# Kernel tuning notes

Hardware: AMD Instinct MI355X
Metric: run time of the kernel (lower is better)

Reference implementation:

```python
import jax, jax.numpy as jnp
import numpy as np

HID = 64; N_LAYERS = 4; N_HEADS = 4; HEAD_DIM = 16; INTER = 32; MAXP = 1024; EPS = 1e-12


def setup_inputs() -> dict:
    key = jax.random.key(0)
    ks = iter(jax.random.split(key, 32))
    rn = lambda shape, s=0.02: jax.random.normal(next(ks), shape, jnp.float32) * s
    B, L = 32, 1024
    return {
        "features": jax.random.normal(next(ks), (B, L, HID), jnp.float32),
        "Wq": rn((N_LAYERS, HID, HID)), "bq": jnp.zeros((N_LAYERS, HID), jnp.float32),
        "Wk": rn((N_LAYERS, HID, HID)), "bk": jnp.zeros((N_LAYERS, HID), jnp.float32),
        "Wv": rn((N_LAYERS, HID, HID)), "bv": jnp.zeros((N_LAYERS, HID), jnp.float32),
        "Wo": rn((N_LAYERS, HID, HID)), "bo": jnp.zeros((N_LAYERS, HID), jnp.float32),
        "ln1_g": jnp.ones((N_LAYERS, HID), jnp.float32), "ln1_b": jnp.zeros((N_LAYERS, HID), jnp.float32),
        "Wi": rn((N_LAYERS, HID, INTER)), "bi": jnp.zeros((N_LAYERS, INTER), jnp.float32),
        "Wd": rn((N_LAYERS, INTER, HID)), "bd": jnp.zeros((N_LAYERS, HID), jnp.float32),
        "ln2_g": jnp.ones((N_LAYERS, HID), jnp.float32), "ln2_b": jnp.zeros((N_LAYERS, HID), jnp.float32),
        "rel_emb": rn((N_LAYERS, 2 * MAXP - 1, HEAD_DIM)),
        "fc_w": rn((HID, 6)), "fc_b": jnp.zeros((6,), jnp.float32),
    }


def _ln(x, g, b):
    m = jnp.mean(x, axis=-1, keepdims=True)
    v = jnp.mean((x - m) ** 2, axis=-1, keepdims=True)
    return (x - m) / jnp.sqrt(v + EPS) * g + b


def reference(features, Wq, bq, Wk, bk, Wv, bv, Wo, bo, ln1_g, ln1_b,
              Wi, bi, Wd, bd, ln2_g, ln2_b, rel_emb, fc_w, fc_b):
    B, L, _ = features.shape
    pos = jnp.arange(L)
    dist_idx = pos[:, None] - pos[None, :] + (MAXP - 1)  # [L, L] in [0, 2*MAXP-2]
    scale = np.float32(1.0 / np.sqrt(HEAD_DIM))

    def heads(t):  # [B,L,HID] -> [B,H,L,D]
        return t.reshape(B, L, N_HEADS, HEAD_DIM).transpose(0, 2, 1, 3)

    x = features
    for i in range(N_LAYERS):
        q = heads(x @ Wq[i] + bq[i])
        k = heads(x @ Wk[i] + bk[i])
        v = heads(x @ Wv[i] + bv[i])
        scores = jnp.einsum("bhld,bhrd->bhlr", q, k)
        pe = rel_emb[i][dist_idx]  # [L, L, D] relative_key positional embedding
        scores = scores + jnp.einsum("bhld,lrd->bhlr", q, pe)
        probs = jax.nn.softmax(scores * scale, axis=-1)
        ctx = jnp.einsum("bhlr,bhrd->bhld", probs, v).transpose(0, 2, 1, 3).reshape(B, L, HID)
        x = _ln(ctx @ Wo[i] + bo[i] + x, ln1_g[i], ln1_b[i])
        inter = jax.nn.gelu(x @ Wi[i] + bi[i], approximate=False)
        x = _ln(inter @ Wd[i] + bd[i] + x, ln2_g[i], ln2_b[i])
    return (x @ fc_w + fc_b)[:, 1:, :]
```

## Files before the change

kernel.cpp:

```cpp
#include <hip/hip_runtime.h>
#include <math.h>

static constexpr int Bc = 32;
static constexpr int Lc = 1024;

typedef _Float16 f16x4 __attribute__((ext_vector_type(4)));
typedef __fp16   h16x2 __attribute__((ext_vector_type(2)));
typedef float    f32x4 __attribute__((ext_vector_type(4)));

#define MFMA16(a, b, c) __builtin_amdgcn_mfma_f32_16x16x16f16((a), (b), (c), 0, 0, 0)

#if __has_builtin(__builtin_amdgcn_exp2f)
#define EXP2(x) __builtin_amdgcn_exp2f(x)
#else
#define EXP2(x) exp2f(x)
#endif

__global__ __launch_bounds__(256) void prep_kernel(
    const float* __restrict__ features, const float* __restrict__ rel,
    const float* __restrict__ Wq, const float* __restrict__ Wk,
    const float* __restrict__ Wv, const float* __restrict__ Wo,
    const float* __restrict__ Wi, const float* __restrict__ Wd,
    _Float16* __restrict__ xh, _Float16* __restrict__ relh,
    _Float16* __restrict__ wt)
{
    int i = blockIdx.x * 256 + threadIdx.x;
    {
        float4 v = ((const float4*)features)[i];
        h16x2 a = __builtin_amdgcn_cvt_pkrtz(v.x, v.y);
        h16x2 b = __builtin_amdgcn_cvt_pkrtz(v.z, v.w);
        f16x4 o; o[0] = a[0]; o[1] = a[1]; o[2] = b[0]; o[3] = b[1];
        ((f16x4*)xh)[i] = o;
    }
    if (i < 32752) {
        float4 v = ((const float4*)rel)[i];
        h16x2 a = __builtin_amdgcn_cvt_pkrtz(v.x, v.y);
        h16x2 b = __builtin_amdgcn_cvt_pkrtz(v.z, v.w);
        f16x4 o; o[0] = a[0]; o[1] = a[1]; o[2] = b[0]; o[3] = b[1];
        ((f16x4*)relh)[i] = o;
    }
    if (i < 65536) {
        int which = i >> 14, r = i & 16383;
        int m = r >> 12, k = (r >> 6) & 63, c = r & 63;
        const float* src = which == 0 ? Wq : which == 1 ? Wk : which == 2 ? Wv : Wo;
        wt[which * 16384 + m * 4096 + c * 64 + k] = (_Float16)src[r];
    } else if (i < 73728) {
        int r = i - 65536;
        int m = r >> 11, k = (r >> 5) & 63, c = r & 31;
        wt[65536 + m * 2048 + c * 64 + k] = (_Float16)Wi[r];
    } else if (i < 81920) {
        int r = i - 73728;
        int m = r >> 11, k = (r >> 6) & 31, c = r & 63;
        wt[73728 + m * 2048 + c * 32 + k] = (_Float16)Wd[r];
    }
}

__global__ __launch_bounds__(256) void qkv_kernel(
    const _Float16* __restrict__ xh,
    const _Float16* __restrict__ qT, const _Float16* __restrict__ kT,
    const _Float16* __restrict__ vT,
    const float* __restrict__ bq, const float* __restrict__ bk,
    const float* __restrict__ bv,
    _Float16* __restrict__ qo, _Float16* __restrict__ ko, _Float16* __restrict__ vt)
{
    const int t = threadIdx.x, wv = t >> 6, lane = t & 63, lo = lane & 15, hi = lane >> 4;
    const int row0 = blockIdx.x * 64 + wv * 16;
    const int b = row0 >> 10, l0 = row0 & 1023;

    f16x4 a[4];
    #pragma unroll
    for (int kk = 0; kk < 4; kk++)
        a[kk] = *(const f16x4*)(xh + (row0 + lo) * 64 + kk * 16 + 4 * hi);

    #pragma unroll
    for (int m = 0; m < 3; m++) {
        const _Float16* WT = m == 0 ? qT : m == 1 ? kT : vT;
        const float* bias  = m == 0 ? bq : m == 1 ? bk : bv;
        #pragma unroll
        for (int h = 0; h < 4; h++) {
            float bb = bias[h * 16 + lo];
            f32x4 acc = { bb, bb, bb, bb };
            #pragma unroll
            for (int kk = 0; kk < 4; kk++) {
                f16x4 bf = *(const f16x4*)(WT + (h * 16 + lo) * 64 + kk * 16 + 4 * hi);
                acc = MFMA16(a[kk], bf, acc);
            }
            int bh = b * 4 + h;
            if (m < 2) {
                _Float16* dst = (m == 0 ? qo : ko) + (bh * Lc + l0 + 4 * hi) * 16 + lo;
                dst[0]  = (_Float16)acc[0];
                dst[16] = (_Float16)acc[1];
                dst[32] = (_Float16)acc[2];
                dst[48] = (_Float16)acc[3];
            } else {
                h16x2 p0 = __builtin_amdgcn_cvt_pkrtz(acc[0], acc[1]);
                h16x2 p1 = __builtin_amdgcn_cvt_pkrtz(acc[2], acc[3]);
                f16x4 o; o[0] = p0[0]; o[1] = p0[1]; o[2] = p1[0]; o[3] = p1[1];
                *(f16x4*)(vt + (bh * 16 + lo) * Lc + l0 + 4 * hi) = o;
            }
        }
    }
}

__global__ __launch_bounds__(256) void layer_kernel(
    const _Float16* __restrict__ qg, const _Float16* __restrict__ kg,
    const _Float16* __restrict__ vtg, const _Float16* __restrict__ relh,
    const float* __restrict__ resid,
    const _Float16* __restrict__ woT, const float* __restrict__ bo,
    const float* __restrict__ g1, const float* __restrict__ b1,
    const _Float16* __restrict__ wiT, const float* __restrict__ bi,
    const _Float16* __restrict__ wdT, const float* __restrict__ bd,
    const float* __restrict__ g2, const float* __restrict__ b2,
    float* __restrict__ xout,
    int doq,
    const _Float16* __restrict__ qT, const _Float16* __restrict__ kT,
    const _Float16* __restrict__ vT,
    const float* __restrict__ bq, const float* __restrict__ bk,
    const float* __restrict__ bv,
    _Float16* __restrict__ qo, _Float16* __restrict__ ko, _Float16* __restrict__ vo)
{
    __shared__ float Tmem[4 * 3328];
    const int tid = threadIdx.x;
    const int wv = tid >> 6, lane = tid & 63;
    const int b  = blockIdx.x & 31;
    const int l0 = (blockIdx.x >> 5) * 64;
    const int bh = b * 4 + wv;
    const int lo = lane & 15, hi = lane >> 4;
    float* wbase = Tmem + wv * 3328;

    {
        const _Float16 qscale = (_Float16)0.36067376022224085f;
        f16x4 qf[4];
        #pragma unroll
        for (int i = 0; i < 4; i++) {
            qf[i] = *(const f16x4*)(qg + (bh * Lc + l0 + 16 * i + lo) * 16 + 4 * hi);
            #pragma unroll
            for (int j = 0; j < 4; j++) qf[i][j] *= qscale;
        }

        const int o = 12 + lo - 4 * hi;

        float* wrE[4]; float* wrO[4]; const float* rdE[4]; const float* rdO[4];
        #pragma unroll
        for (int i = 0; i < 4; i++) {
            float* ring = wbase + i * 832;
            const int phiE = 16 * (i & 1);
            const int phiO = 16 - phiE;
            wrE[i] = ring + lo * 52 + phiE + 4 * hi;
            wrO[i] = ring + lo * 52 + phiO + 4 * hi;
            rdE[i] = ring + lo * 52 + phiE + o;
            rdO[i] = ring + lo * 52 + phiO + o;
        }

        const _Float16* rbase = relh + 4 * hi;
        auto ldrel = [&](int row) {
            row = row > 2046 ? 2046 : row;
            return *(const f16x4*)(rbase + row * 16);
        };
        auto t_store = [&](f16x4 rf, f16x4 q, float* wr, bool mir) {
            f32x4 z = { 0.f, 0.f, 0.f, 0.f };
            f32x4 tt = MFMA16(rf, q, z);
            *(f32x4*)(wr) = tt;
            if (mir) *(f32x4*)(wr + 32) = tt;
        };

        f16x4 P[6];
        #pragma unroll
        for (int k = 0; k < 6; k++) P[k] = ldrel(l0 + 16 * k + lo);
        #pragma unroll
        for (int i = 0; i < 4; i++) {
            t_store(P[i],     qf[i], wrE[i], (i & 1) == 0);
            t_store(P[i + 1], qf[i], wrO[i], (i & 1) == 1);
        }
        f16x4 rc0 = P[2], rc1 = P[3], rc2 = P[4], rc3 = P[5];
        int rrow = l0 + 96 + lo;

        f32x4 si[4];
        #pragma unroll
        for (int i = 0; i < 4; i++) {
            const float* rd = rdE[i];
            si[i][0] = rd[3]; si[i][1] = rd[2]; si[i][2] = rd[1]; si[i][3] = rd[0];
        }

        const _Float16* kp = kg  + (bh * Lc + 1008 + lo) * 16 + 4 * hi;
        const _Float16* vp = vtg + (bh * 16 + lo) * Lc + 1008 + 4 * hi;
        f16x4 kf0 = *(const f16x4*)kp;
        f16x4 vf0 = *(const f16x4*)vp;
        kp -= 256; vp -= 16;
        f16x4 kf1 = *(const f16x4*)kp;
        f16x4 vf1 = *(const f16x4*)vp;

        f32x4 ot[4], d[4];
        #pragma unroll
        for (int i = 0; i < 4; i++) {
            ot[i] = f32x4{ 0.f, 0.f, 0.f, 0.f };
            d[i]  = f32x4{ 0.f, 0.f, 0.f, 0.f };
        }

        #pragma unroll 2
        for (int t = 0; t < 64; ++t) {
            kp -= 256; vp -= 16;
            f16x4 kf2 = *(const f16x4*)kp;
            f16x4 vf2 = *(const f16x4*)vp;
            f16x4 r4 = ldrel(rrow); rrow += 16;

            f32x4 s[4];
            #pragma unroll
            for (int i = 0; i < 4; i++)
                s[i] = MFMA16(kf0, qf[i], si[i]);

            float e[4][4];
            #pragma unroll
            for (int i = 0; i < 4; i++)
                #pragma unroll
                for (int j = 0; j < 4; j++) {
                    e[i][j] = EXP2(s[i][j]);
                    d[i][j] += e[i][j];
                }

            t_store(rc0, qf[0], (t & 1) ? wrO[0] : wrE[0], (t & 1) == 0);
            t_store(rc1, qf[1], (t & 1) ? wrO[1] : wrE[1], (t & 1) == 1);
            t_store(rc2, qf[2], (t & 1) ? wrO[2] : wrE[2], (t & 1) == 0);
            t_store(rc3, qf[3], (t & 1) ? wrO[3] : wrE[3], (t & 1) == 1);

            #pragma unroll
            for (int i = 0; i < 4; i++) {
                const float* rd = (t & 1) ? rdE[i] : rdO[i];
                si[i][0] = rd[3]; si[i][1] = rd[2]; si[i][2] = rd[1]; si[i][3] = rd[0];
            }

            #pragma unroll
            for (int i = 0; i < 4; i++) {
                h16x2 pa = __builtin_amdgcn_cvt_pkrtz(e[i][0], e[i][1]);
                h16x2 pb = __builtin_amdgcn_cvt_pkrtz(e[i][2], e[i][3]);
                f16x4 pf; pf[0] = pa[0]; pf[1] = pa[1]; pf[2] = pb[0]; pf[3] = pb[1];
                ot[i] = MFMA16(vf0, pf, ot[i]);
            }

            kf0 = kf1; kf1 = kf2;
            vf0 = vf1; vf1 = vf2;
            rc0 = rc1; rc1 = rc2; rc2 = rc3; rc3 = r4;
        }

        _Float16* ctxw = (_Float16*)wbase;
        #pragma unroll
        for (int i = 0; i < 4; i++) {
            float den = (d[i][0] + d[i][1]) + (d[i][2] + d[i][3]);
            den += __shfl_xor(den, 16);
            den += __shfl_xor(den, 32);
            const float inv = 1.f / den;
            h16x2 o0 = __builtin_amdgcn_cvt_pkrtz(ot[i][0] * inv, ot[i][1] * inv);
            h16x2 o1 = __builtin_amdgcn_cvt_pkrtz(ot[i][2] * inv, ot[i][3] * inv);
            f16x4 o4; o4[0] = o0[0]; o4[1] = o0[1]; o4[2] = o1[0]; o4[3] = o1[1];
            *(f16x4*)(ctxw + (16 * i + lo) * 16 + 4 * hi) = o4;
        }
    }
    __syncthreads();

    const _Float16* ctxs = (const _Float16*)Tmem;
    const int row0g = b * Lc + l0 + wv * 16;

    f16x4 a[4];
    #pragma unroll
    for (int kk = 0; kk < 4; kk++)
        a[kk] = *(const f16x4*)(ctxs + kk * 6656 + (wv * 16 + lo) * 16 + 4 * hi);

    float c1[4][4];
    #pragma unroll
    for (int w = 0; w < 4; w++) {
        float bb = bo[w * 16 + lo];
        f32x4 acc;
        #pragma unroll
        for (int j = 0; j < 4; j++)
            acc[j] = bb + resid[(row0g + 4 * hi + j) * 64 + w * 16 + lo];
        #pragma unroll
        for (int kk = 0; kk < 4; kk++) {
            f16x4 bf = *(const f16x4*)(woT + (w * 16 + lo) * 64 + kk * 16 + 4 * hi);
            acc = MFMA16(a[kk], bf, acc);
        }
        #pragma unroll
        for (int j = 0; j < 4; j++) c1[w][j] = acc[j];
    }

    float x1[4][4];
    {
        float gg[4], bb2[4];
        #pragma unroll
        for (int w = 0; w < 4; w++) { gg[w] = g1[w * 16 + lo]; bb2[w] = b1[w * 16 + lo]; }
        #pragma unroll
        for (int j = 0; j < 4; j++) {
            float s = c1[0][j] + c1[1][j] + c1[2][j] + c1[3][j];
            float q = c1[0][j]*c1[0][j] + c1[1][j]*c1[1][j] + c1[2][j]*c1[2][j] + c1[3][j]*c1[3][j];
            #pragma unroll
            for (int off = 1; off < 16; off <<= 1) { s += __shfl_xor(s, off); q += __shfl_xor(q, off); }
            float m  = s * (1.f / 64.f);
            float vr = q * (1.f / 64.f) - m * m;
            float rs = rsqrtf(vr + 1e-12f);
            #pragma unroll
            for (int w = 0; w < 4; w++) x1[w][j] = (c1[w][j] - m) * rs * gg[w] + bb2[w];
        }
    }

    _Float16* xsp = (_Float16*)(wbase + 512);
    _Float16* isp = (_Float16*)(wbase + 512 + 544);

    #pragma unroll
    for (int w = 0; w < 4; w++)
        #pragma unroll
        for (int j = 0; j < 4; j++)
            xsp[(4 * hi + j) * 68 + w * 16 + lo] = (_Float16)x1[w][j];
    f16x4 a2[4];
    #pragma unroll
    for (int kk = 0; kk < 4; kk++)
        a2[kk] = *(const f16x4*)(xsp + lo * 68 + kk * 16 + 4 * hi);

    float it[2][4];
    #pragma unroll
    for (int w = 0; w < 2; w++) {
        float bb = bi[w * 16 + lo];
        f32x4 acc = { bb, bb, bb, bb };
        #pragma unroll
        for (int kk = 0; kk < 4; kk++) {
            f16x4 bf = *(const f16x4*)(wiT + (w * 16 + lo) * 64 + kk * 16 + 4 * hi);
            acc = MFMA16(a2[kk], bf, acc);
        }
        #pragma unroll
        for (int j = 0; j < 4; j++) {
            float v = acc[j];
            it[w][j] = 0.5f * v * (1.f + erff(v * 0.70710678118654752f));
        }
    }

    #pragma unroll
    for (int w = 0; w < 2; w++)
        #pragma unroll
        for (int j = 0; j < 4; j++)
            isp[(4 * hi + j) * 36 + w * 16 + lo] = (_Float16)it[w][j];
    f16x4 a3[2];
    #pragma unroll
    for (int kk = 0; kk < 2; kk++)
        a3[kk] = *(const f16x4*)(isp + lo * 36 + kk * 16 + 4 * hi);

    float c2[4][4];
    #pragma unroll
    for (int w = 0; w < 4; w++) {
        float bb = bd[w * 16 + lo];
        f32x4 acc;
        #pragma unroll
        for (int j = 0; j < 4; j++) acc[j] = bb + x1[w][j];
        #pragma unroll
        for (int kk = 0; kk < 2; kk++) {
            f16x4 bf = *(const f16x4*)(wdT + (w * 16 + lo) * 32 + kk * 16 + 4 * hi);
            acc = MFMA16(a3[kk], bf, acc);
        }
        #pragma unroll
        for (int j = 0; j < 4; j++) c2[w][j] = acc[j];
    }

    float x2[4][4];
    {
        float gg[4], bb2[4];
        #pragma unroll
        for (int w = 0; w < 4; w++) { gg[w] = g2[w * 16 + lo]; bb2[w] = b2[w * 16 + lo]; }
        #pragma unroll
        for (int j = 0; j < 4; j++) {
            float s = c2[0][j] + c2[1][j] + c2[2][j] + c2[3][j];
            float q = c2[0][j]*c2[0][j] + c2[1][j]*c2[1][j] + c2[2][j]*c2[2][j] + c2[3][j]*c2[3][j];
            #pragma unroll
            for (int off = 1; off < 16; off <<= 1) { s += __shfl_xor(s, off); q += __shfl_xor(q, off); }
            float m  = s * (1.f / 64.f);
            float vr = q * (1.f / 64.f) - m * m;
            float rs = rsqrtf(vr + 1e-12f);
            #pragma unroll
            for (int w = 0; w < 4; w++) {
                float xv = (c2[w][j] - m) * rs * gg[w] + bb2[w];
                x2[w][j] = xv;
                xout[(row0g + 4 * hi + j) * 64 + w * 16 + lo] = xv;
            }
        }
    }

    if (!doq) return;

    #pragma unroll
    for (int w = 0; w < 4; w++)
        #pragma unroll
        for (int j = 0; j < 4; j++)
            xsp[(4 * hi + j) * 68 + w * 16 + lo] = (_Float16)x2[w][j];
    f16x4 aq[4];
    #pragma unroll
    for (int kk = 0; kk < 4; kk++)
        aq[kk] = *(const f16x4*)(xsp + lo * 68 + kk * 16 + 4 * hi);

    const int bb_ = row0g >> 10, l0q = row0g & 1023;
    #pragma unroll
    for (int m = 0; m < 3; m++) {
        const _Float16* WT = m == 0 ? qT : m == 1 ? kT : vT;
        const float* bias  = m == 0 ? bq : m == 1 ? bk : bv;
        #pragma unroll
        for (int h = 0; h < 4; h++) {
            float bb = bias[h * 16 + lo];
            f32x4 acc = { bb, bb, bb, bb };
            #pragma unroll
            for (int kk = 0; kk < 4; kk++) {
                f16x4 bf = *(const f16x4*)(WT + (h * 16 + lo) * 64 + kk * 16 + 4 * hi);
                acc = MFMA16(aq[kk], bf, acc);
            }
            int bhn = bb_ * 4 + h;
            if (m < 2) {
                _Float16* dst = (m == 0 ? qo : ko) + (bhn * Lc + l0q + 4 * hi) * 16 + lo;
                dst[0]  = (_Float16)acc[0];
                dst[16] = (_Float16)acc[1];
                dst[32] = (_Float16)acc[2];
                dst[48] = (_Float16)acc[3];
            } else {
                h16x2 p0 = __builtin_amdgcn_cvt_pkrtz(acc[0], acc[1]);
                h16x2 p1 = __builtin_amdgcn_cvt_pkrtz(acc[2], acc[3]);
                f16x4 o; o[0] = p0[0]; o[1] = p0[1]; o[2] = p1[0]; o[3] = p1[1];
                *(f16x4*)(vo + (bhn * 16 + lo) * Lc + l0q + 4 * hi) = o;
            }
        }
    }
}

__global__ __launch_bounds__(256) void final_kernel(
    const float* __restrict__ x, const float* __restrict__ fcw,
    const float* __restrict__ fcb, float* __restrict__ out)
{
    int idx = blockIdx.x * 256 + threadIdx.x;
    if (idx >= Bc * 1023 * 6) return;
    int j = idx % 6;
    int rest = idx / 6;
    int l = rest % 1023 + 1;
    int b = rest / 1023;
    const float* xr = x + (b * Lc + l) * 64;
    float acc = fcb[j];
    for (int k = 0; k < 64; ++k) acc += xr[k] * fcw[k * 6 + j];
    out[idx] = acc;
}

extern "C" void kernel_launch(void* const* d_in, const int* in_sizes, int n_in,
                              void* d_out, int out_size, void* d_ws, size_t ws_size,
                              hipStream_t stream)
{
    (void)in_sizes; (void)n_in; (void)out_size; (void)ws_size;
    const float* features = (const float*)d_in[0];
    const float* Wq  = (const float*)d_in[1];
    const float* bq  = (const float*)d_in[2];
    const float* Wk  = (const float*)d_in[3];
    const float* bk  = (const float*)d_in[4];
    const float* Wv  = (const float*)d_in[5];
    const float* bv  = (const float*)d_in[6];
    const float* Wo  = (const float*)d_in[7];
    const float* bo  = (const float*)d_in[8];
    const float* g1  = (const float*)d_in[9];
    const float* b1  = (const float*)d_in[10];
    const float* Wi  = (const float*)d_in[11];
    const float* bi  = (const float*)d_in[12];
    const float* Wd  = (const float*)d_in[13];
    const float* bd  = (const float*)d_in[14];
    const float* g2  = (const float*)d_in[15];
    const float* b2  = (const float*)d_in[16];
    const float* rel = (const float*)d_in[17];
    const float* fcw = (const float*)d_in[18];
    const float* fcb = (const float*)d_in[19];
    float* out = (float*)d_out;

    char* ws = (char*)d_ws;
    float*    xbuf = (float*)(ws);
    _Float16* qh1  = (_Float16*)(ws + ( 8u << 20));
    _Float16* xh   = qh1;
    _Float16* kh1  = (_Float16*)(ws + (12u << 20));
    _Float16* vt1  = (_Float16*)(ws + (16u << 20));
    _Float16* qh0  = (_Float16*)(ws + (20u << 20));
    _Float16* kh0  = (_Float16*)(ws + (24u << 20));
    _Float16* vt0  = (_Float16*)(ws + (28u << 20));
    _Float16* relh = (_Float16*)(ws + (32u << 20));
    _Float16* wt   = (_Float16*)(ws + (32u << 20) + (512u << 10));

    prep_kernel<<<2048, 256, 0, stream>>>(features, rel, Wq, Wk, Wv, Wo, Wi, Wd,
                                          xh, relh, wt);
    qkv_kernel<<<512, 256, 0, stream>>>(xh,
        wt, wt + 16384, wt + 32768, bq, bk, bv, qh0, kh0, vt0);

    for (int i = 0; i < 4; ++i) {
        const float* resid = (i == 0) ? features : xbuf;
        const int ni = (i < 3) ? (i + 1) : 3;
        const _Float16* qin = (i & 1) ? qh1 : qh0;
        const _Float16* kin = (i & 1) ? kh1 : kh0;
        const _Float16* vin = (i & 1) ? vt1 : vt0;
        _Float16* qout = (i & 1) ? qh0 : qh1;
        _Float16* kout = (i & 1) ? kh0 : kh1;
        _Float16* vout = (i & 1) ? vt0 : vt1;

        layer_kernel<<<512, 256, 0, stream>>>(qin, kin, vin,
            relh + i * 2047 * 16, resid,
            wt + 49152 + i * 4096, bo + i * 64, g1 + i * 64, b1 + i * 64,
            wt + 65536 + i * 2048, bi + i * 32,
            wt + 73728 + i * 2048, bd + i * 64, g2 + i * 64, b2 + i * 64,
            xbuf,
            (i < 3) ? 1 : 0,
            wt + ni * 4096, wt + 16384 + ni * 4096, wt + 32768 + ni * 4096,
            bq + ni * 64, bk + ni * 64, bv + ni * 64,
            qout, kout, vout);
    }
    final_kernel<<<768, 256, 0, stream>>>(xbuf, fcw, fcb, out);
}
```

Measured before the change: 262.8 us.

## Halve query rows per attention block to double grid size

Each layer block now handles 32 query rows instead of 64, so each wave carries two query tiles instead of four, shared memory is halved, and the grid grows from 512 to 1024 blocks. The aim is better occupancy and more parallelism on the many CUs, with lower register and LDS pressure per block. The cost is twice the K/V and relative-embedding streaming per query, less MFMA work per loaded K/V fragment, and only two of four waves doing the post-attention MLP/projection phase.

Measured after the change: 291.0 us. +10.7%, slower.

```diff
diff --git a/kernel.cpp b/kernel.cpp
--- a/kernel.cpp
+++ b/kernel.cpp
@@ -119,20 +119,20 @@
     const float* __restrict__ bv,
     _Float16* __restrict__ qo, _Float16* __restrict__ ko, _Float16* __restrict__ vo)
 {
-    __shared__ float Tmem[4 * 3328];
+    __shared__ float Tmem[4 * 1664];
     const int tid = threadIdx.x;
     const int wv = tid >> 6, lane = tid & 63;
     const int b  = blockIdx.x & 31;
-    const int l0 = (blockIdx.x >> 5) * 64;
+    const int l0 = (blockIdx.x >> 5) * 32;
     const int bh = b * 4 + wv;
     const int lo = lane & 15, hi = lane >> 4;
-    float* wbase = Tmem + wv * 3328;
+    float* wbase = Tmem + wv * 1664;
 
     {
         const _Float16 qscale = (_Float16)0.36067376022224085f;
-        f16x4 qf[4];
-        #pragma unroll
-        for (int i = 0; i < 4; i++) {
+        f16x4 qf[2];
+        #pragma unroll
+        for (int i = 0; i < 2; i++) {
             qf[i] = *(const f16x4*)(qg + (bh * Lc + l0 + 16 * i + lo) * 16 + 4 * hi);
             #pragma unroll
             for (int j = 0; j < 4; j++) qf[i][j] *= qscale;
@@ -140,9 +140,9 @@
 
         const int o = 12 + lo - 4 * hi;
 
-        float* wrE[4]; float* wrO[4]; const float* rdE[4]; const float* rdO[4];
-        #pragma unroll
-        for (int i = 0; i < 4; i++) {
+        float* wrE[2]; float* wrO[2]; const float* rdE[2]; const float* rdO[2];
+        #pragma unroll
+        for (int i = 0; i < 2; i++) {
             float* ring = wbase + i * 832;
             const int phiE = 16 * (i & 1);
             const int phiO = 16 - phiE;
@@ -164,20 +164,19 @@
             if (mir) *(f32x4*)(wr + 32) = tt;
         };
 
-        f16x4 P[6];
-        #pragma unroll
-        for (int k = 0; k < 6; k++) P[k] = ldrel(l0 + 16 * k + lo);
-        #pragma unroll
-        for (int i = 0; i < 4; i++) {
-            t_store(P[i],     qf[i], wrE[i], (i & 1) == 0);
-            t_store(P[i + 1], qf[i], wrO[i], (i & 1) == 1);
-        }
-        f16x4 rc0 = P[2], rc1 = P[3], rc2 = P[4], rc3 = P[5];
-        int rrow = l0 + 96 + lo;
-
-        f32x4 si[4];
-        #pragma unroll
-        for (int i = 0; i < 4; i++) {
+        f16x4 P[4];
+        #pragma unroll
+        for (int k = 0; k < 4; k++) P[k] = ldrel(l0 + 16 * k + lo);
+        t_store(P[0], qf[0], wrE[0], true);
+        t_store(P[1], qf[0], wrO[0], false);
+        t_store(P[1], qf[1], wrE[1], false);
+        t_store(P[2], qf[1], wrO[1], true);
+        f16x4 rc0 = P[2], rc1 = P[3];
+        int rrow = l0 + 64 + lo;
+
+        f32x4 si[2];
+        #pragma unroll
+        for (int i = 0; i < 2; i++) {
             const float* rd = rdE[i];
             si[i][0] = rd[3]; si[i][1] = rd[2]; si[i][2] = rd[1]; si[i][3] = rd[0];
         }
@@ -190,9 +189,9 @@
         f16x4 kf1 = *(const f16x4*)kp;
         f16x4 vf1 = *(const f16x4*)vp;
 
-        f32x4 ot[4], d[4];
-        #pragma unroll
-        for (int i = 0; i < 4; i++) {
+        f32x4 ot[2], d[2];
+        #pragma unroll
+        for (int i = 0; i < 2; i++) {
             ot[i] = f32x4{ 0.f, 0.f, 0.f, 0.f };
             d[i]  = f32x4{ 0.f, 0.f, 0.f, 0.f };
         }
@@ -202,49 +201,48 @@
             kp -= 256; vp -= 16;
             f16x4 kf2 = *(const f16x4*)kp;
             f16x4 vf2 = *(const f16x4*)vp;
-            f16x4 r4 = ldrel(rrow); rrow += 16;
-
-            f32x4 s[4];
-            #pragma unroll
-            for (int i = 0; i < 4; i++)
-                s[i] = MFMA16(kf0, qf[i], si[i]);
-
-            float e[4][4];
-            #pragma unroll
-            for (int i = 0; i < 4; i++)
-                #pragma unroll
-                for (int j = 0; j < 4; j++) {
-                    e[i][j] = EXP2(s[i][j]);
-                    d[i][j] += e[i][j];
-                }
+            f16x4 r2 = ldrel(rrow); rrow += 16;
+
+            f32x4 s0 = MFMA16(kf0, qf[0], si[0]);
+            f32x4 s1 = MFMA16(kf0, qf[1], si[1]);
+
+            float e0[4], e1[4];
+            #pragma unroll
+            for (int j = 0; j < 4; j++) {
+                e0[j] = EXP2(s0[j]); d[0][j] += e0[j];
+                e1[j] = EXP2(s1[j]); d[1][j] += e1[j];
+            }
 
             t_store(rc0, qf[0], (t & 1) ? wrO[0] : wrE[0], (t & 1) == 0);
             t_store(rc1, qf[1], (t & 1) ? wrO[1] : wrE[1], (t & 1) == 1);
-            t_store(rc2, qf[2], (t & 1) ? wrO[2] : wrE[2], (t & 1) == 0);
-            t_store(rc3, qf[3], (t & 1) ? wrO[3] : wrE[3], (t & 1) == 1);
-
-            #pragma unroll
-            for (int i = 0; i < 4; i++) {
+
+            #pragma unroll
+            for (int i = 0; i < 2; i++) {
                 const float* rd = (t & 1) ? rdE[i] : rdO[i];
                 si[i][0] = rd[3]; si[i][1] = rd[2]; si[i][2] = rd[1]; si[i][3] = rd[0];
             }
 
-            #pragma unroll
-            for (int i = 0; i < 4; i++) {
-                h16x2 pa = __builtin_amdgcn_cvt_pkrtz(e[i][0], e[i][1]);
-                h16x2 pb = __builtin_amdgcn_cvt_pkrtz(e[i][2], e[i][3]);
+            {
+                h16x2 pa = __builtin_amdgcn_cvt_pkrtz(e0[0], e0[1]);
+                h16x2 pb = __builtin_amdgcn_cvt_pkrtz(e0[2], e0[3]);
                 f16x4 pf; pf[0] = pa[0]; pf[1] = pa[1]; pf[2] = pb[0]; pf[3] = pb[1];
-                ot[i] = MFMA16(vf0, pf, ot[i]);
+                ot[0] = MFMA16(vf0, pf, ot[0]);
+            }
+            {
+                h16x2 pa = __builtin_amdgcn_cvt_pkrtz(e1[0], e1[1]);
+                h16x2 pb = __builtin_amdgcn_cvt_pkrtz(e1[2], e1[3]);
+                f16x4 pf; pf[0] = pa[0]; pf[1] = pa[1]; pf[2] = pb[0]; pf[3] = pb[1];
+                ot[1] = MFMA16(vf0, pf, ot[1]);
             }
 
             kf0 = kf1; kf1 = kf2;
             vf0 = vf1; vf1 = vf2;
-            rc0 = rc1; rc1 = rc2; rc2 = rc3; rc3 = r4;
+            rc0 = rc1; rc1 = r2;
         }
 
         _Float16* ctxw = (_Float16*)wbase;
         #pragma unroll
-        for (int i = 0; i < 4; i++) {
+        for (int i = 0; i < 2; i++) {
             float den = (d[i][0] + d[i][1]) + (d[i][2] + d[i][3]);
             den += __shfl_xor(den, 16);
             den += __shfl_xor(den, 32);
@@ -256,14 +254,16 @@
         }
     }
     __syncthreads();
-
-    const _Float16* ctxs = (const _Float16*)Tmem;
-    const int row0g = b * Lc + l0 + wv * 16;
+    if (wv >= 2) return;
+
+    const int tw = wv;
+    const int row0g = b * Lc + l0 + tw * 16;
 
     f16x4 a[4];
     #pragma unroll
     for (int kk = 0; kk < 4; kk++)
-        a[kk] = *(const f16x4*)(ctxs + kk * 6656 + (wv * 16 + lo) * 16 + 4 * hi);
+        a[kk] = *(const f16x4*)((const _Float16*)(Tmem + kk * 1664)
+                                + (tw * 16 + lo) * 16 + 4 * hi);
 
     float c1[4][4];
     #pragma unroll
@@ -301,8 +301,8 @@
         }
     }
 
-    _Float16* xsp = (_Float16*)(wbase + 512);
-    _Float16* isp = (_Float16*)(wbase + 512 + 544);
+    _Float16* xsp = (_Float16*)(Tmem + (2 + tw) * 1664 + 256);
+    _Float16* isp = xsp + 1088;
 
     #pragma unroll
     for (int w = 0; w < 4; w++)
@@ -392,7 +392,7 @@
     for (int kk = 0; kk < 4; kk++)
         aq[kk] = *(const f16x4*)(xsp + lo * 68 + kk * 16 + 4 * hi);
 
-    const int bb_ = row0g >> 10, l0q = row0g & 1023;
+    const int l0q = l0 + tw * 16;
     #pragma unroll
     for (int m = 0; m < 3; m++) {
         const _Float16* WT = m == 0 ? qT : m == 1 ? kT : vT;
@@ -406,7 +406,7 @@
                 f16x4 bf = *(const f16x4*)(WT + (h * 16 + lo) * 64 + kk * 16 + 4 * hi);
                 acc = MFMA16(aq[kk], bf, acc);
             }
-            int bhn = bb_ * 4 + h;
+            int bhn = b * 4 + h;
             if (m < 2) {
                 _Float16* dst = (m == 0 ? qo : ko) + (bhn * Lc + l0q + 4 * hi) * 16 + lo;
                 dst[0]  = (_Float16)acc[0];
@@ -493,7 +493,7 @@
         _Float16* kout = (i & 1) ? kh0 : kh1;
         _Float16* vout = (i & 1) ? vt0 : vt1;
 
-        layer_kernel<<<512, 256, 0, stream>>>(qin, kin, vin,
+        layer_kernel<<<1024, 256, 0, stream>>>(qin, kin, vin,
             relh + i * 2047 * 16, resid,
             wt + 49152 + i * 4096, bo + i * 64, g1 + i * 64, b1 + i * 64,
             wt + 65536 + i * 2048, bi + i * 32,
```

## Split attention key range across two wave groups with fp16 score ring

Applied to the files above, without the earlier changes.

Doubles the layer kernel to 512 threads so two groups of four waves each process half the key range (split-K attention). Partial outputs and denominators are combined through shared memory. The relative-position ring buffer moves from fp32 to fp16 to halve LDS use, and the denominator is accumulated with packed fdot2. This trades extra LDS traffic, a reduction step and lower bias precision for more waves in flight on the serial key loop.

Measured after the change: 365.6 us. 1.39x slower.

```diff
diff --git a/kernel.cpp b/kernel.cpp
--- a/kernel.cpp
+++ b/kernel.cpp
@@ -15,6 +15,15 @@
 #else
 #define EXP2(x) exp2f(x)
 #endif
+
+__device__ inline float fdot2_acc(h16x2 a, float c) {
+#if __has_builtin(__builtin_amdgcn_fdot2)
+    h16x2 one2 = { (__fp16)1.f, (__fp16)1.f };
+    return __builtin_amdgcn_fdot2(a, one2, c, false);
+#else
+    return c + (float)a[0] + (float)a[1];
+#endif
+}
 
 __global__ __launch_bounds__(256) void prep_kernel(
     const float* __restrict__ features, const float* __restrict__ rel,
@@ -102,7 +111,7 @@
     }
 }
 
-__global__ __launch_bounds__(256) void layer_kernel(
+__global__ __launch_bounds__(512) void layer_kernel(
     const _Float16* __restrict__ qg, const _Float16* __restrict__ kg,
     const _Float16* __restrict__ vtg, const _Float16* __restrict__ relh,
     const float* __restrict__ resid,
@@ -119,14 +128,15 @@
     const float* __restrict__ bv,
     _Float16* __restrict__ qo, _Float16* __restrict__ ko, _Float16* __restrict__ vo)
 {
-    __shared__ float Tmem[4 * 3328];
+    __shared__ float Tmem[8 * 1664];
     const int tid = threadIdx.x;
     const int wv = tid >> 6, lane = tid & 63;
     const int b  = blockIdx.x & 31;
     const int l0 = (blockIdx.x >> 5) * 64;
-    const int bh = b * 4 + wv;
+    const int hd = wv & 3, rh = wv >> 2;
+    const int bh = b * 4 + hd;
     const int lo = lane & 15, hi = lane >> 4;
-    float* wbase = Tmem + wv * 3328;
+    float* wbase = Tmem + wv * 1664;
 
     {
         const _Float16 qscale = (_Float16)0.36067376022224085f;
@@ -139,11 +149,13 @@
         }
 
         const int o = 12 + lo - 4 * hi;
-
-        float* wrE[4]; float* wrO[4]; const float* rdE[4]; const float* rdO[4];
+        _Float16* ringh = (_Float16*)wbase;
+
+        _Float16* wrE[4]; _Float16* wrO[4];
+        const _Float16* rdE[4]; const _Float16* rdO[4];
         #pragma unroll
         for (int i = 0; i < 4; i++) {
-            float* ring = wbase + i * 832;
+            _Float16* ring = ringh + i * 832;
             const int phiE = 16 * (i & 1);
             const int phiO = 16 - phiE;
             wrE[i] = ring + lo * 52 + phiE + 4 * hi;
@@ -157,48 +169,52 @@
             row = row > 2046 ? 2046 : row;
             return *(const f16x4*)(rbase + row * 16);
         };
-        auto t_store = [&](f16x4 rf, f16x4 q, float* wr, bool mir) {
+        auto t_store = [&](f16x4 rf, f16x4 q, _Float16* wr, bool mir) {
             f32x4 z = { 0.f, 0.f, 0.f, 0.f };
             f32x4 tt = MFMA16(rf, q, z);
-            *(f32x4*)(wr) = tt;
-            if (mir) *(f32x4*)(wr + 32) = tt;
+            h16x2 t0 = __builtin_amdgcn_cvt_pkrtz(tt[0], tt[1]);
+            h16x2 t1 = __builtin_amdgcn_cvt_pkrtz(tt[2], tt[3]);
+            f16x4 tv; tv[0] = t0[0]; tv[1] = t0[1]; tv[2] = t1[0]; tv[3] = t1[1];
+            *(f16x4*)(wr) = tv;
+            if (mir) *(f16x4*)(wr + 32) = tv;
         };
 
+        const int jb = l0 + 512 * rh;
         f16x4 P[6];
         #pragma unroll
-        for (int k = 0; k < 6; k++) P[k] = ldrel(l0 + 16 * k + lo);
+        for (int k = 0; k < 6; k++) P[k] = ldrel(jb + 16 * k + lo);
         #pragma unroll
         for (int i = 0; i < 4; i++) {
             t_store(P[i],     qf[i], wrE[i], (i & 1) == 0);
             t_store(P[i + 1], qf[i], wrO[i], (i & 1) == 1);
         }
         f16x4 rc0 = P[2], rc1 = P[3], rc2 = P[4], rc3 = P[5];
-        int rrow = l0 + 96 + lo;
+        int rrow = jb + 96 + lo;
 
         f32x4 si[4];
         #pragma unroll
         for (int i = 0; i < 4; i++) {
-            const float* rd = rdE[i];
-            si[i][0] = rd[3]; si[i][1] = rd[2]; si[i][2] = rd[1]; si[i][3] = rd[0];
-        }
-
-        const _Float16* kp = kg  + (bh * Lc + 1008 + lo) * 16 + 4 * hi;
-        const _Float16* vp = vtg + (bh * 16 + lo) * Lc + 1008 + 4 * hi;
+            const _Float16* rd = rdE[i];
+            si[i][0] = (float)rd[3]; si[i][1] = (float)rd[2];
+            si[i][2] = (float)rd[1]; si[i][3] = (float)rd[0];
+        }
+
+        const int rstart = 1008 - 512 * rh;
+        const _Float16* kp = kg  + (bh * Lc + rstart + lo) * 16 + 4 * hi;
+        const _Float16* vp = vtg + (bh * 16 + lo) * Lc + rstart + 4 * hi;
         f16x4 kf0 = *(const f16x4*)kp;
         f16x4 vf0 = *(const f16x4*)vp;
         kp -= 256; vp -= 16;
         f16x4 kf1 = *(const f16x4*)kp;
         f16x4 vf1 = *(const f16x4*)vp;
 
-        f32x4 ot[4], d[4];
-        #pragma unroll
-        for (int i = 0; i < 4; i++) {
-            ot[i] = f32x4{ 0.f, 0.f, 0.f, 0.f };
-            d[i]  = f32x4{ 0.f, 0.f, 0.f, 0.f };
-        }
+        f32x4 ot[4];
+        float dd[4] = { 0.f, 0.f, 0.f, 0.f };
+        #pragma unroll
+        for (int i = 0; i < 4; i++) ot[i] = f32x4{ 0.f, 0.f, 0.f, 0.f };
 
         #pragma unroll 2
-        for (int t = 0; t < 64; ++t) {
+        for (int t = 0; t < 32; ++t) {
             kp -= 256; vp -= 16;
             f16x4 kf2 = *(const f16x4*)kp;
             f16x4 vf2 = *(const f16x4*)vp;
@@ -209,14 +225,16 @@
             for (int i = 0; i < 4; i++)
                 s[i] = MFMA16(kf0, qf[i], si[i]);
 
-            float e[4][4];
-            #pragma unroll
-            for (int i = 0; i < 4; i++)
-                #pragma unroll
-                for (int j = 0; j < 4; j++) {
-                    e[i][j] = EXP2(s[i][j]);
-                    d[i][j] += e[i][j];
-                }
+            h16x2 pa_[4], pb_[4];
+            #pragma unroll
+            for (int i = 0; i < 4; i++) {
+                float e0 = EXP2(s[i][0]), e1 = EXP2(s[i][1]);
+                float e2 = EXP2(s[i][2]), e3 = EXP2(s[i][3]);
+                pa_[i] = __builtin_amdgcn_cvt_pkrtz(e0, e1);
+                pb_[i] = __builtin_amdgcn_cvt_pkrtz(e2, e3);
+                dd[i] = fdot2_acc(pa_[i], dd[i]);
+                dd[i] = fdot2_acc(pb_[i], dd[i]);
+            }
 
             t_store(rc0, qf[0], (t & 1) ? wrO[0] : wrE[0], (t & 1) == 0);
             t_store(rc1, qf[1], (t & 1) ? wrO[1] : wrE[1], (t & 1) == 1);
@@ -225,15 +243,16 @@
 
             #pragma unroll
             for (int i = 0; i < 4; i++) {
-                const float* rd = (t & 1) ? rdE[i] : rdO[i];
-                si[i][0] = rd[3]; si[i][1] = rd[2]; si[i][2] = rd[1]; si[i][3] = rd[0];
+                const _Float16* rd = (t & 1) ? rdE[i] : rdO[i];
+                si[i][0] = (float)rd[3]; si[i][1] = (float)rd[2];
+                si[i][2] = (float)rd[1]; si[i][3] = (float)rd[0];
             }
 
             #pragma unroll
             for (int i = 0; i < 4; i++) {
-                h16x2 pa = __builtin_amdgcn_cvt_pkrtz(e[i][0], e[i][1]);
-                h16x2 pb = __builtin_amdgcn_cvt_pkrtz(e[i][2], e[i][3]);
-                f16x4 pf; pf[0] = pa[0]; pf[1] = pa[1]; pf[2] = pb[0]; pf[3] = pb[1];
+                f16x4 pf;
+                pf[0] = pa_[i][0]; pf[1] = pa_[i][1];
+                pf[2] = pb_[i][0]; pf[3] = pb_[i][1];
                 ot[i] = MFMA16(vf0, pf, ot[i]);
             }
 
@@ -242,28 +261,36 @@
             rc0 = rc1; rc1 = rc2; rc2 = rc3; rc3 = r4;
         }
 
-        _Float16* ctxw = (_Float16*)wbase;
+        float* ctxf = wbase;
+        float* denf = wbase + 1024;
         #pragma unroll
         for (int i = 0; i < 4; i++) {
-            float den = (d[i][0] + d[i][1]) + (d[i][2] + d[i][3]);
+            float den = dd[i];
             den += __shfl_xor(den, 16);
             den += __shfl_xor(den, 32);
-            const float inv = 1.f / den;
-            h16x2 o0 = __builtin_amdgcn_cvt_pkrtz(ot[i][0] * inv, ot[i][1] * inv);
-            h16x2 o1 = __builtin_amdgcn_cvt_pkrtz(ot[i][2] * inv, ot[i][3] * inv);
-            f16x4 o4; o4[0] = o0[0]; o4[1] = o0[1]; o4[2] = o1[0]; o4[3] = o1[1];
-            *(f16x4*)(ctxw + (16 * i + lo) * 16 + 4 * hi) = o4;
+            if (lane < 16) denf[16 * i + lane] = den;
+            *(f32x4*)(ctxf + (16 * i + lo) * 16 + 4 * hi) = ot[i];
         }
     }
     __syncthreads();
-
-    const _Float16* ctxs = (const _Float16*)Tmem;
-    const int row0g = b * Lc + l0 + wv * 16;
+    if (wv >= 4) return;
+
+    const int tw = wv;
+    const int row0g = b * Lc + l0 + tw * 16;
 
     f16x4 a[4];
     #pragma unroll
-    for (int kk = 0; kk < 4; kk++)
-        a[kk] = *(const f16x4*)(ctxs + kk * 6656 + (wv * 16 + lo) * 16 + 4 * hi);
+    for (int kk = 0; kk < 4; kk++) {
+        const float* rA = Tmem + kk * 1664;
+        const float* rB = Tmem + (kk + 4) * 1664;
+        const int row = tw * 16 + lo;
+        float inv = 1.f / (rA[1024 + row] + rB[1024 + row]);
+        f32x4 cA = *(const f32x4*)(rA + row * 16 + 4 * hi);
+        f32x4 cB = *(const f32x4*)(rB + row * 16 + 4 * hi);
+        h16x2 p0 = __builtin_amdgcn_cvt_pkrtz((cA[0] + cB[0]) * inv, (cA[1] + cB[1]) * inv);
+        h16x2 p1 = __builtin_amdgcn_cvt_pkrtz((cA[2] + cB[2]) * inv, (cA[3] + cB[3]) * inv);
+        a[kk][0] = p0[0]; a[kk][1] = p0[1]; a[kk][2] = p1[0]; a[kk][3] = p1[1];
+    }
 
     float c1[4][4];
     #pragma unroll
@@ -301,8 +328,8 @@
         }
     }
 
-    _Float16* xsp = (_Float16*)(wbase + 512);
-    _Float16* isp = (_Float16*)(wbase + 512 + 544);
+    _Float16* xsp = (_Float16*)(Tmem + (4 + tw) * 1664 + 1088);
+    _Float16* isp = (_Float16*)(Tmem + tw * 1664 + 1088);
 
     #pragma unroll
     for (int w = 0; w < 4; w++)
@@ -392,7 +419,7 @@
     for (int kk = 0; kk < 4; kk++)
         aq[kk] = *(const f16x4*)(xsp + lo * 68 + kk * 16 + 4 * hi);
 
-    const int bb_ = row0g >> 10, l0q = row0g & 1023;
+    const int l0q = l0 + tw * 16;
     #pragma unroll
     for (int m = 0; m < 3; m++) {
         const _Float16* WT = m == 0 ? qT : m == 1 ? kT : vT;
@@ -406,7 +433,7 @@
                 f16x4 bf = *(const f16x4*)(WT + (h * 16 + lo) * 64 + kk * 16 + 4 * hi);
                 acc = MFMA16(aq[kk], bf, acc);
             }
-            int bhn = bb_ * 4 + h;
+            int bhn = b * 4 + h;
             if (m < 2) {
                 _Float16* dst = (m == 0 ? qo : ko) + (bhn * Lc + l0q + 4 * hi) * 16 + lo;
                 dst[0]  = (_Float16)acc[0];
@@ -493,7 +520,7 @@
         _Float16* kout = (i & 1) ? kh0 : kh1;
         _Float16* vout = (i & 1) ? vt0 : vt1;
 
-        layer_kernel<<<512, 256, 0, stream>>>(qin, kin, vin,
+        layer_kernel<<<512, 512, 0, stream>>>(qin, kin, vin,
             relh + i * 2047 * 16, resid,
             wt + 49152 + i * 4096, bo + i * 64, g1 + i * 64, b1 + i * 64,
             wt + 65536 + i * 2048, bi + i * 32,
```
